# Kernel tuning notes

Hardware: AMD Instinct MI355X
Metric: run time of the kernel (lower is better)

## Reference

```python
import jax, jax.numpy as jnp
import numpy as np

T_STEPS = 16384  # sequence length T
N_DIM = 256      # input channels n
M_DIM = 512      # hidden/reservoir size m
K_MEM = 511      # memory rows K (addresses are 0..K, row 0 = 'no memory op')
L_OUT = 256      # output dims L


def setup_inputs() -> dict:
    key = jax.random.key(0)
    ks = jax.random.split(key, 10)
    s_ih = 1.0 / np.sqrt(N_DIM)
    s_hh = 1.0 / np.sqrt(M_DIM)
    X = jax.random.normal(ks[0], (T_STEPS, N_DIM), jnp.float32)
    h0 = jnp.zeros((M_DIM,), jnp.float32)  # init_state = zeros(m)
    # torch.nn.GRU parameters (single layer): weight_ih [3m, n], weight_hh [3m, m]
    W_ih = jax.random.normal(ks[1], (3 * M_DIM, N_DIM), jnp.float32) * s_ih
    W_hh = jax.random.normal(ks[2], (3 * M_DIM, M_DIM), jnp.float32) * s_hh
    b_ih = jax.random.normal(ks[3], (3 * M_DIM,), jnp.float32) * s_hh
    b_hh = jax.random.normal(ks[4], (3 * M_DIM,), jnp.float32) * s_hh
    # C_: Linear(m, K+1) -> memory address logits
    C_w = jax.random.normal(ks[5], (K_MEM + 1, M_DIM), jnp.float32) * s_hh
    C_b = jax.random.normal(ks[6], (K_MEM + 1,), jnp.float32) * s_hh
    # V_: Linear(m, L) -> outputs
    V_w = jax.random.normal(ks[7], (L_OUT, M_DIM), jnp.float32) * s_hh
    V_b = jax.random.normal(ks[8], (L_OUT,), jnp.float32) * s_hh
    return {"X": X, "h0": h0, "W_ih": W_ih, "W_hh": W_hh, "b_ih": b_ih,
            "b_hh": b_hh, "C_w": C_w, "C_b": C_b, "V_w": V_w, "V_b": V_b}


def reference(X, h0, W_ih, W_hh, b_ih, b_hh, C_w, C_b, V_w, V_b):
    m = h0.shape[0]
    n_addr = C_b.shape[0]  # K + 1

    def step(carry, x):
        h, M, written = carry
        # GRU cell (torch semantics)
        gi = W_ih @ x + b_ih          # [3m]
        gh = W_hh @ h + b_hh          # [3m]
        i_r, i_z, i_n = jnp.split(gi, 3)
        h_r, h_z, h_n = jnp.split(gh, 3)
        r = jax.nn.sigmoid(i_r + h_r)
        z = jax.nn.sigmoid(i_z + h_z)
        ng = jnp.tanh(i_n + r * h_n)
        h_new = (1.0 - z) * ng + z * h
        # discrete memory addressing via argmax over C_(h)
        logits = C_w @ h_new + C_b    # [K+1]
        q = jnp.argmax(logits)
        mem_q = M[q]                  # gather (read before write)
        has_entry = written[q] & (q > 0)
        # if address already written: read memory, replacing h
        h_out = jnp.where(has_entry, mem_q, h_new)
        # if address new (and > 0): write h into memory
        do_write = (q > 0) & jnp.logical_not(written[q])
        write_val = jnp.where(do_write, h_new, mem_q)  # no-op write otherwise
        M = M.at[q].set(write_val)
        written = written.at[q].set(written[q] | (q > 0))
        return (h_out, M, written), h_out

    M0 = jnp.zeros((n_addr, m), X.dtype)       # q_0 = 0 -> memory starts empty
    written0 = jnp.zeros((n_addr,), jnp.bool_)
    _, H = jax.lax.scan(step, (h0, M0, written0), X)  # H: [T, m]
    Y = H @ V_w.T + V_b                          # [T, L]
    return Y
```

## Files before the change

### kernel.cpp

```cpp
#include <hip/hip_runtime.h>
#include <stdint.h>

#define T_STEPS 16384
#define NDIM 256
#define MDIM 512
#define KP1 512
#define LOUT 256
#define G 16
#define TPB 256
#define NBLK 256

typedef unsigned long long u64;
typedef unsigned int u32;

constexpr size_t OFF_GH    = 0;
constexpr size_t OFF_GHS   = 512ull * 1536;
constexpr size_t OFF_M     = OFF_GHS + 1536;
constexpr size_t OFF_RING  = OFF_M + 512ull * 512;
constexpr size_t OFF_H     = OFF_RING + 4ull * 1536;
constexpr size_t OFF_VWT   = OFF_H + 16384ull * 512;
constexpr size_t OFF_FLAGS = OFF_VWT + 512ull * 256;

__device__ __forceinline__ float ld_cohf(const float* p) {
  return __hip_atomic_load(p, __ATOMIC_RELAXED, __HIP_MEMORY_SCOPE_AGENT);
}
__device__ __forceinline__ void st_cohf(float* p, float v) {
  __hip_atomic_store(p, v, __ATOMIC_RELAXED, __HIP_MEMORY_SCOPE_AGENT);
}
__device__ __forceinline__ u64 ld_flag(const u64* p) {
  return __hip_atomic_load(p, __ATOMIC_RELAXED, __HIP_MEMORY_SCOPE_AGENT);
}
__device__ __forceinline__ void st_flag_rel(u64* p, u64 v) {
  __hip_atomic_store(p, v, __ATOMIC_RELEASE, __HIP_MEMORY_SCOPE_AGENT);
}
__device__ __forceinline__ void st_flag_rlx(u64* p, u64 v) {
  __hip_atomic_store(p, v, __ATOMIC_RELAXED, __HIP_MEMORY_SCOPE_AGENT);
}

__device__ __forceinline__ u64 ld64_sc0(const u64* p) {
  u64 v;
  asm volatile("global_load_dwordx2 %0, %1, off sc0\n\t"
               "s_waitcnt vmcnt(0)"
               : "=&v"(v) : "v"(p) : "memory");
  return v;
}
__device__ __forceinline__ void st64_sc0(u64* p, u64 v) {
  asm volatile("global_store_dwordx2 %0, %1, off sc0" :: "v"(p), "v"(v) : "memory");
}
__device__ __forceinline__ void drain_vm() {
  asm volatile("s_waitcnt vmcnt(0)" ::: "memory");
}

#define HWREG_XCC_ID ((31u << 11) | 20u)
__device__ __forceinline__ u32 xcc_id() {
  return (u32)__builtin_amdgcn_s_getreg(HWREG_XCC_ID) & 0xFu;
}

__device__ __forceinline__ float sigm(float x) {
  return __builtin_amdgcn_rcpf(1.0f + __expf(-x));
}
__device__ __forceinline__ float tanh_(float x) {
  return 1.0f - 2.0f * __builtin_amdgcn_rcpf(__expf(2.0f * x) + 1.0f);
}

template<int CTRL>
__device__ __forceinline__ u32 dppmax(u32 v) {
  u32 t = (u32)__builtin_amdgcn_update_dpp(0, (int)v, CTRL, 0xf, 0xf, true);
  return v > t ? v : t;
}
__device__ __forceinline__ u32 wave_max_u32(u32 v) {
  v = dppmax<0x111>(v);
  v = dppmax<0x112>(v);
  v = dppmax<0x114>(v);
  v = dppmax<0x118>(v);
  v = dppmax<0x142>(v);
  v = dppmax<0x143>(v);
  return (u32)__builtin_amdgcn_readlane((int)v, 63);
}
__device__ __forceinline__ u32 row16_max_u32(u32 v) {
  v = dppmax<0x111>(v);
  v = dppmax<0x112>(v);
  v = dppmax<0x114>(v);
  v = dppmax<0x118>(v);
  return (u32)__builtin_amdgcn_readlane((int)v, 15);
}

__global__ __launch_bounds__(TPB, 1) void dmm_main(
    const float* __restrict__ X, const float* __restrict__ h0,
    const float* __restrict__ W_ih, const float* __restrict__ W_hh,
    const float* __restrict__ b_ih, const float* __restrict__ b_hh,
    const float* __restrict__ C_w, const float* __restrict__ C_b,
    float* __restrict__ ws)
{
  const int tid = threadIdx.x;
  const int w   = tid >> 6;
  const int l   = tid & 63;

  float* GH   = ws + OFF_GH;
  float* GHS  = ws + OFF_GHS;
  float* Mrow = ws + OFF_M;
  float* RING = ws + OFF_RING;
  float* H    = ws + OFF_H;
  u64*   F    = (u64*)(ws + OFF_FLAGS);

  u32* Ecnt = (u32*)Mrow;
  u64* Tst  = (u64*)(Mrow + 16);
  u64* Md   = (u64*)(Mrow + 64);

  __shared__ __align__(16) float hnew[MDIM];
  __shared__ __align__(16) float red[96 * 36];
  __shared__ u32 written[KP1];
  __shared__ u32 bcw;
  __shared__ int s_i;

  if (tid == 0) {
    u32 xcc = xcc_id();
    int widx = -1;
    if (xcc == 0) {
      u32 r = __hip_atomic_fetch_add(Ecnt, 1u, __ATOMIC_RELAXED,
                                     __HIP_MEMORY_SCOPE_AGENT);
      if (r < (u32)G) widx = (int)r;
    } else if (blockIdx.x < G) {
      int guard = 0; u32 c;
      do {
        c = __hip_atomic_load(Ecnt, __ATOMIC_RELAXED, __HIP_MEMORY_SCOPE_AGENT);
      } while (c < (u32)G && ++guard < (1 << 12));
      if (c < (u32)G) {
        u32 r = __hip_atomic_fetch_add(Ecnt, 1u, __ATOMIC_RELAXED,
                                       __HIP_MEMORY_SCOPE_AGENT);
        if (r < (u32)G) widx = (int)r;
      }
    }
    s_i = widx;
  }
  __syncthreads();
  const int b = s_i;
  __syncthreads();
  if (b < 0) return;

  __shared__ int s_good;
  if (tid == 0) s_good = 1;
  __syncthreads();
  for (int r = 1; r <= 8; ++r) {
    if (tid == 0 && s_good) {
      drain_vm();
      st64_sc0(&Tst[b], (u64)r);
    }
    if (w == 0 && s_good) {
      int guard = 0;
      for (;;) {
        u64 v = (u64)r;
        if (l < G) v = ld64_sc0(&Tst[l]);
        bool ok = (l >= G) || (v >= (u64)r);
        if (__ballot((int)ok) == ~0ull) break;
        if (++guard > (1 << 12)) { if (l == 0) s_good = 0; break; }
      }
    }
    __syncthreads();
  }
  if (tid == 0)
    __hip_atomic_store(&Md[b], 2ull | (u64)s_good, __ATOMIC_RELEASE,
                       __HIP_MEMORY_SCOPE_AGENT);
  if (w == 0) {
    int guard = 0, moderes = 0;
    for (;;) {
      u64 v = 3ull;
      if (l < G) v = __hip_atomic_load(&Md[l], __ATOMIC_ACQUIRE,
                                       __HIP_MEMORY_SCOPE_AGENT);
      bool ok = (l >= G) || ((v & 2ull) != 0);
      if (__ballot((int)ok) == ~0ull) {
        u64 bm = __ballot((int)((v & 1ull) != 0));
        moderes = (bm == ~0ull) ? 1 : 0;
        break;
      }
      if (++guard > (1 << 20)) { moderes = 0; break; }
    }
    if (l == 0) s_i = moderes;
  }
  __syncthreads();
  const bool SC0F = (s_i != 0);
  const int GSTEP = SC0F ? (1 << 12) : (1 << 22);


  const int pw   = (w >= 1) ? (w - 1) : 0;
  const int rloc = pw * 32 + (l >> 4) * 8;
  float wih[8][16];
  {
    int rbase = 96 * b + rloc;
    int cbase = 16 * (l & 15);
#pragma unroll
    for (int i = 0; i < 8; i++)
#pragma unroll
      for (int k = 0; k < 16; k++)
        wih[i][k] = W_ih[(size_t)(rbase + i) * NDIM + cbase + k];
  }
  float bihr[8];
#pragma unroll
  for (int i = 0; i < 8; i++) bihr[i] = b_ih[96 * b + rloc + i];

  float cw[4][16];
  {
    int rbase = 32 * b + w * 8 + (l >> 5) * 4;
    int cbase = 16 * (l & 31);
#pragma unroll
    for (int i = 0; i < 4; i++)
#pragma unroll
      for (int k = 0; k < 16; k++)
        cw[i][k] = C_w[(size_t)(rbase + i) * MDIM + cbase + k];
  }

  for (int i = tid; i < KP1; i += TPB) written[i] = 0u;
  if (tid == 0) bcw = 0u;
  hnew[tid]       = h0[tid];
  hnew[tid + 256] = h0[tid + 256];
  __syncthreads();

  float xreg[16];
  auto prefetchX = [&](int s) {
    int cbase = 16 * (l & 15);
#pragma unroll
    for (int k = 0; k < 16; k++) xreg[k] = X[(size_t)s * NDIM + cbase + k];
  };

  auto produce_gi = [&](int s) {
    float p[8];
#pragma unroll
    for (int i = 0; i < 8; i++) {
      float a = 0.f;
#pragma unroll
      for (int k = 0; k < 16; k++) a = fmaf(wih[i][k], xreg[k], a);
      p[i] = a;
    }
#pragma unroll
    for (int off = 1; off <= 8; off <<= 1) {
#pragma unroll
      for (int i = 0; i < 8; i++) p[i] += __shfl_xor(p[i], off, 64);
    }
    if ((l & 15) == 0) {
      float* dst = &RING[(size_t)(s & 3) * 1536 + 96 * b + rloc];
#pragma unroll
      for (int i = 0; i < 8; i++) st_cohf(&dst[i], p[i] + bihr[i]);
    }
  };

  auto compute_gh = [&](float* dst) {
    int cb = 16 * (l & 31);
    float hr[16];
#pragma unroll
    for (int k = 0; k < 16; k += 4) *(float4*)&hr[k] = *(const float4*)&hnew[cb + k];
    int rb = 96 * b + w * 24 + (l >> 5) * 12;
    float p[12];
#pragma unroll
    for (int i = 0; i < 12; i++) {
      float a = 0.f;
      const float* wr = &W_hh[(size_t)(rb + i) * MDIM + cb];
#pragma unroll
      for (int k = 0; k < 16; k++) a = fmaf(wr[k], hr[k], a);
      p[i] = a;
    }
    int rl = w * 24 + (l >> 5) * 12;
    int lc = l & 31;
#pragma unroll
    for (int i = 0; i < 12; i++) red[(rl + i) * 36 + lc] = p[i];
    __syncthreads();
    if (tid < 96) {
      float a = 0.f;
#pragma unroll
      for (int k = 0; k < 32; k += 4) {
        float4 v = *(const float4*)&red[tid * 36 + k];
        a += v.x + v.y + v.z + v.w;
      }
      a += b_hh[96 * b + tid];
      st_cohf(&dst[96 * b + tid], a);
    }
    __syncthreads();
  };

  if (w >= 1) {
    prefetchX(0); produce_gi(0);
    prefetchX(1); produce_gi(1);
    prefetchX(2); produce_gi(2);
    prefetchX(3);
  }
  __syncthreads();
  compute_gh(GHS);
  if (tid == 0) st_flag_rel(&F[b], 1ull);
  if (w == 0) {
    int guard = 0;
    for (;;) {
      u64 v = (l < G) ? ld_flag(&F[l]) : 1ull;
      if (__ballot((int)(v == 1ull)) == ~0ull) break;
      if (++guard > (1 << 22)) break;
    }
  }
  __syncthreads();

  const float* ghsrc = GHS;
  bool prevReadHit = false;
  int  qprev = 0;

  for (int t = 0; t < T_STEPS; ++t) {
    float g0 = ld_cohf(&ghsrc[tid]);
    float g1 = ld_cohf(&ghsrc[tid + 256]);
    float g2 = ld_cohf(&ghsrc[512 + tid]);
    float g3 = ld_cohf(&ghsrc[512 + tid + 256]);
    float g4 = ld_cohf(&ghsrc[1024 + tid]);
    float g5 = ld_cohf(&ghsrc[1024 + tid + 256]);
    float m0 = 0.f, m1 = 0.f;
    if (prevReadHit) {
      m0 = ld_cohf(&Mrow[(size_t)qprev * 512 + tid]);
      m1 = ld_cohf(&Mrow[(size_t)qprev * 512 + tid + 256]);
    }
    const float* gi = &RING[(size_t)(t & 3) * 1536];
    float i0 = ld_cohf(&gi[tid]);
    float i1 = ld_cohf(&gi[tid + 256]);
    float i2 = ld_cohf(&gi[512 + tid]);
    float i3 = ld_cohf(&gi[512 + tid + 256]);
    float i4 = ld_cohf(&gi[1024 + tid]);
    float i5 = ld_cohf(&gi[1024 + tid + 256]);

    if (prevReadHit && b == 0) {
      __builtin_nontemporal_store(m0, &H[(size_t)(t - 1) * 512 + tid]);
      __builtin_nontemporal_store(m1, &H[(size_t)(t - 1) * 512 + tid + 256]);
    }

    float hp0 = prevReadHit ? m0 : hnew[tid];
    float hp1 = prevReadHit ? m1 : hnew[tid + 256];
    float r0 = sigm(i0 + g0), r1 = sigm(i1 + g1);
    float z0 = sigm(i2 + g2), z1 = sigm(i3 + g3);
    float n0 = tanh_(fmaf(r0, g4, i4)), n1 = tanh_(fmaf(r1, g5, i5));
    float hn0 = fmaf(z0, hp0 - n0, n0);
    float hn1 = fmaf(z1, hp1 - n1, n1);
    hnew[tid]       = hn0;
    hnew[tid + 256] = hn1;
    __syncthreads();

    {
      int cb = 16 * (l & 31);
      float hr[16];
#pragma unroll
      for (int k = 0; k < 16; k += 4) *(float4*)&hr[k] = *(const float4*)&hnew[cb + k];
      float p0 = 0.f, p1 = 0.f, p2 = 0.f, p3 = 0.f;
#pragma unroll
      for (int k = 0; k < 16; k++) {
        p0 = fmaf(cw[0][k], hr[k], p0);
        p1 = fmaf(cw[1][k], hr[k], p1);
        p2 = fmaf(cw[2][k], hr[k], p2);
        p3 = fmaf(cw[3][k], hr[k], p3);
      }
      int rl = w * 8 + (l >> 5) * 4;
      int lc = l & 31;
      red[(rl + 0) * 36 + lc] = p0;
      red[(rl + 1) * 36 + lc] = p1;
      red[(rl + 2) * 36 + lc] = p2;
      red[(rl + 3) * 36 + lc] = p3;
    }
    __syncthreads();

    u64 ownkey = 0;
    if (w <= 1) {
      u32 ord = 0;
      if (l < 32) {
        const float4* rp = (const float4*)&red[l * 36];
        float4 v0 = rp[0], v1 = rp[1], v2 = rp[2], v3 = rp[3];
        float4 v4 = rp[4], v5 = rp[5], v6 = rp[6], v7 = rp[7];
        double d0 = ((double)v0.x + (double)v0.y) + ((double)v0.z + (double)v0.w);
        double d1 = ((double)v1.x + (double)v1.y) + ((double)v1.z + (double)v1.w);
        double d2 = ((double)v2.x + (double)v2.y) + ((double)v2.z + (double)v2.w);
        double d3 = ((double)v3.x + (double)v3.y) + ((double)v3.z + (double)v3.w);
        double d4 = ((double)v4.x + (double)v4.y) + ((double)v4.z + (double)v4.w);
        double d5 = ((double)v5.x + (double)v5.y) + ((double)v5.z + (double)v5.w);
        double d6 = ((double)v6.x + (double)v6.y) + ((double)v6.z + (double)v6.w);
        double d7 = ((double)v7.x + (double)v7.y) + ((double)v7.z + (double)v7.w);
        double a = (((d0 + d1) + (d2 + d3)) + ((d4 + d5) + (d6 + d7)))
                 + (double)C_b[32 * b + l];
        float af = (float)a;
        u32 bits = __float_as_uint(af);
        ord = (bits & 0x80000000u) ? ~bits : (bits | 0x80000000u);
      }
      u32 maxord = wave_max_u32(ord);
      u64 mask = __ballot((int)(ord == maxord));
      int lane = __builtin_ctzll(mask);
      u64 key41 = ((u64)maxord << 9) | (u64)(511 - (32 * b + lane));
      if (tid == 64) {
        u64 fv = ((u64)(t + 1) << 41) | key41;
        u64* fp = &F[16 + (size_t)(t & 1) * 16 + b];
        if (SC0F) st64_sc0(fp, fv); else st_flag_rlx(fp, fv);
      }
      ownkey = key41;
    }

    if (w >= 1 && t + 3 < T_STEPS) {
      produce_gi(t + 3);
      if (t + 4 < T_STEPS) prefetchX(t + 4);
    }

    u32 info;
    if (w == 0) {
      const bool need = (l < G) && (l != b);
      const u64* fp = &F[16 + (size_t)(t & 1) * 16 + l];
      u64 v = 0;
      if (SC0F) {
        int guard = 0;
        for (;;) {
          if (need) v = ld64_sc0(fp);
          bool ok = !need || ((v >> 41) == (u64)(t + 1));
          if (__ballot((int)ok) == ~0ull) break;
          if (++guard > GSTEP) break;
        }
      } else {
        u64 vp = need ? ld_flag(fp) : 0;
        int guard = 0;
        for (;;) {
          u64 vn = need ? ld_flag(fp) : 0;
          bool ok = !need || ((vp >> 41) == (u64)(t + 1));
          if (__ballot((int)ok) == ~0ull) { v = vp; break; }
          vp = vn;
          if (++guard > GSTEP) { v = vp; break; }
        }
      }
      u64 key = (l < G) ? ((l == b) ? ownkey : (v & ((1ull << 41) - 1))) : 0;
      u32 o = (u32)(key >> 9);
      u32 maxo = row16_max_u32(o);
      u32 cand = (o == maxo && l < G) ? (u32)(key & 511u) : 0u;
      u32 best = row16_max_u32(cand);
      int q = 511 - (int)best;
      u32 vinfo = 0;
      if (l == 0) {
        u32 wr = written[q];
        u32 fresh = (q > 0 && wr == 0u) ? 1u : 0u;
        u32 rhit  = (q > 0 && wr != 0u) ? 1u : 0u;
        if (fresh) written[q] = 1u;
        vinfo = (u32)q | (fresh << 16) | (rhit << 17);
      }
      vinfo = (u32)__builtin_amdgcn_readfirstlane((int)vinfo);
      info = vinfo;
      if (l == 0)
        __hip_atomic_store(&bcw, (vinfo << 4) | ((u32)(t + 1) & 0xFu),
                           __ATOMIC_RELEASE, __HIP_MEMORY_SCOPE_WORKGROUP);
    } else {
      u32 v;
      int guard = 0;
      for (;;) {
        v = __hip_atomic_load(&bcw, __ATOMIC_ACQUIRE, __HIP_MEMORY_SCOPE_WORKGROUP);
        if ((v & 0xFu) == ((u32)(t + 1) & 0xFu)) break;
        if (++guard > (1 << 25)) break;
      }
      info = v >> 4;
    }
    int  q     = (int)(info & 0xFFFFu);
    bool fresh = (info >> 16) & 1u;
    bool rhit  = (info >> 17) & 1u;

    if (!rhit) {
      if (b == 0) {
        __builtin_nontemporal_store(hnew[tid], &H[(size_t)t * 512 + tid]);
        __builtin_nontemporal_store(hnew[tid + 256], &H[(size_t)t * 512 + tid + 256]);
      }
      float* dst;
      if (fresh) {
        if (tid < 32) st_cohf(&Mrow[(size_t)q * 512 + 32 * b + tid], hnew[32 * b + tid]);
        dst = &GH[(size_t)q * 1536];
      } else {
        dst = GHS;
      }
      compute_gh(dst);
      if (tid == 0) {
        u64* fp = &F[48 + (size_t)(t & 1) * 16 + b];
        if (SC0F) { drain_vm(); st64_sc0(fp, (u64)(t + 1)); }
        else st_flag_rel(fp, (u64)(t + 1));
      }
      if (w == 0) {
        int guard = 0;
        for (;;) {
          u64 v;
          const u64* fp = &F[48 + (size_t)(t & 1) * 16 + l];
          if (l < G) v = SC0F ? ld64_sc0(fp) : ld_flag(fp);
          else v = (u64)(t + 1);
          bool ok = (l >= G) || (v == (u64)(t + 1));
          if (__ballot((int)ok) == ~0ull) break;
          if (++guard > GSTEP) break;
        }
      }
      __syncthreads();
      ghsrc = dst;
      prevReadHit = false;
    } else {
      ghsrc = &GH[(size_t)q * 1536];
      prevReadHit = true;
      qprev = q;
    }
  }

  if (prevReadHit && b == 0) {
    float a = ld_cohf(&Mrow[(size_t)qprev * 512 + tid]);
    float c = ld_cohf(&Mrow[(size_t)qprev * 512 + tid + 256]);
    __builtin_nontemporal_store(a, &H[(size_t)(T_STEPS - 1) * 512 + tid]);
    __builtin_nontemporal_store(c, &H[(size_t)(T_STEPS - 1) * 512 + tid + 256]);
  }
}

__global__ void vw_transpose(const float* __restrict__ Vw, float* __restrict__ VwT) {
  int idx = blockIdx.x * 256 + threadIdx.x;
  if (blockIdx.x == 0) {
    float* M0 = VwT - (OFF_VWT - OFF_M);
    M0[threadIdx.x] = 0.f;
  }
  int kk = idx >> 8, ll = idx & 255;
  VwT[idx] = Vw[(size_t)ll * MDIM + kk];
}

__global__ __launch_bounds__(256) void y_gemm(const float* __restrict__ Hm,
                                              const float* __restrict__ VwT,
                                              const float* __restrict__ Vb,
                                              float* __restrict__ Y) {
  int t0 = blockIdx.x * 16;
  int tid = threadIdx.x;
  __shared__ __align__(16) float hs[16 * MDIM];
  for (int i = tid; i < 16 * MDIM; i += 256)
    hs[i] = Hm[(size_t)t0 * MDIM + i];
  __syncthreads();
  float acc[16];
  float vb = Vb[tid];
#pragma unroll
  for (int r = 0; r < 16; r++) acc[r] = vb;
  for (int k = 0; k < MDIM; k += 4) {
    float v0 = VwT[(size_t)(k + 0) * LOUT + tid];
    float v1 = VwT[(size_t)(k + 1) * LOUT + tid];
    float v2 = VwT[(size_t)(k + 2) * LOUT + tid];
    float v3 = VwT[(size_t)(k + 3) * LOUT + tid];
#pragma unroll
    for (int r = 0; r < 16; r++) {
      float4 h4 = *(const float4*)&hs[r * MDIM + k];
      acc[r] = fmaf(h4.x, v0, fmaf(h4.y, v1, fmaf(h4.z, v2, fmaf(h4.w, v3, acc[r]))));
    }
  }
#pragma unroll
  for (int r = 0; r < 16; r++)
    Y[(size_t)(t0 + r) * LOUT + tid] = acc[r];
}

extern "C" void kernel_launch(void* const* d_in, const int* in_sizes, int n_in,
                              void* d_out, int out_size, void* d_ws, size_t ws_size,
                              hipStream_t stream) {
  const float* X    = (const float*)d_in[0];
  const float* h0   = (const float*)d_in[1];
  const float* W_ih = (const float*)d_in[2];
  const float* W_hh = (const float*)d_in[3];
  const float* b_ih = (const float*)d_in[4];
  const float* b_hh = (const float*)d_in[5];
  const float* C_w  = (const float*)d_in[6];
  const float* C_b  = (const float*)d_in[7];
  const float* V_w  = (const float*)d_in[8];
  const float* V_b  = (const float*)d_in[9];
  float* ws  = (float*)d_ws;
  float* VwT = ws + OFF_VWT;
  float* Hm  = ws + OFF_H;

  hipLaunchKernelGGL(vw_transpose, dim3(512), dim3(256), 0, stream, V_w, VwT);
  hipLaunchKernelGGL(dmm_main, dim3(NBLK), dim3(TPB), 0, stream,
                     X, h0, W_ih, W_hh, b_ih, b_hh, C_w, C_b, ws);
  hipLaunchKernelGGL(y_gemm, dim3(T_STEPS / 16), dim3(256), 0, stream,
                     Hm, VwT, V_b, (float*)d_out);
}
```

Baseline: 40.87 ms.

## Use sc0 inline-asm loads/stores and padded flag slots for cross-block sync

On the SC0F path, the per-step loads of gate and memory rows are bundled into one inline-asm block of sc0 loads with a single waitcnt, and stores use sc0 stores followed by explicit drains. The argmax and completion flags move to padded slots (stride 16 u64) placed in the otherwise-unused GH row 0 region, which vw_transpose now zeroes. X prefetches become nontemporal loads. The aim is to cut coherence latency and false sharing in the per-step inter-block handshakes, at the cost of relying on ordering assumptions for the sc0 cache-bypass semantics and extra vmcnt drains.

```diff
diff --git a/kernel.cpp b/kernel.cpp
--- a/kernel.cpp
+++ b/kernel.cpp
@@ -47,9 +47,35 @@
 __device__ __forceinline__ void st64_sc0(u64* p, u64 v) {
   asm volatile("global_store_dwordx2 %0, %1, off sc0" :: "v"(p), "v"(v) : "memory");
 }
+__device__ __forceinline__ void stf_sc0(float* p, float v) {
+  asm volatile("global_store_dword %0, %1, off sc0" :: "v"(p), "v"(v) : "memory");
+}
 __device__ __forceinline__ void drain_vm() {
   asm volatile("s_waitcnt vmcnt(0)" ::: "memory");
 }
+
+#define BUNDLE_SC0()                                                 \
+      asm volatile(                                                  \
+        "global_load_dword %0, %14, off sc0\n\t"                     \
+        "global_load_dword %1, %14, off offset:1024 sc0\n\t"         \
+        "global_load_dword %2, %14, off offset:2048 sc0\n\t"         \
+        "global_load_dword %3, %14, off offset:3072 sc0\n\t"         \
+        "global_load_dword %4, %15, off sc0\n\t"                     \
+        "global_load_dword %5, %15, off offset:1024 sc0\n\t"         \
+        "global_load_dword %6, %16, off sc0\n\t"                     \
+        "global_load_dword %7, %16, off offset:1024 sc0\n\t"         \
+        "global_load_dword %8, %16, off offset:2048 sc0\n\t"         \
+        "global_load_dword %9, %16, off offset:3072 sc0\n\t"         \
+        "global_load_dword %10, %17, off sc0\n\t"                    \
+        "global_load_dword %11, %17, off offset:1024 sc0\n\t"        \
+        "global_load_dword %12, %18, off sc0\n\t"                    \
+        "global_load_dword %13, %18, off offset:1024 sc0\n\t"        \
+        "s_waitcnt vmcnt(0)"                                         \
+        : "=&v"(g0), "=&v"(g1), "=&v"(g2), "=&v"(g3), "=&v"(g4), "=&v"(g5), \
+          "=&v"(i0), "=&v"(i1), "=&v"(i2), "=&v"(i3), "=&v"(i4), "=&v"(i5), \
+          "=&v"(m0), "=&v"(m1)                                       \
+        : "v"(pg0), "v"(pg4), "v"(pi0), "v"(pi4), "v"(pm0)           \
+        : "memory")
 
 #define HWREG_XCC_ID ((31u << 11) | 20u)
 __device__ __forceinline__ u32 xcc_id() {
@@ -102,6 +128,8 @@
   float* RING = ws + OFF_RING;
   float* H    = ws + OFF_H;
   u64*   F    = (u64*)(ws + OFF_FLAGS);
+  u64*   FB1  = (u64*)(ws + OFF_GH);
+  u64*   FC1  = (u64*)(ws + OFF_GH) + 512;
 
   u32* Ecnt = (u32*)Mrow;
   u64* Tst  = (u64*)(Mrow + 16);
@@ -218,8 +246,14 @@
   float xreg[16];
   auto prefetchX = [&](int s) {
     int cbase = 16 * (l & 15);
-#pragma unroll
-    for (int k = 0; k < 16; k++) xreg[k] = X[(size_t)s * NDIM + cbase + k];
+    const float* xp = &X[(size_t)s * NDIM + cbase];
+    if (SC0F) {
+#pragma unroll
+      for (int k = 0; k < 16; k++) xreg[k] = __builtin_nontemporal_load(&xp[k]);
+    } else {
+#pragma unroll
+      for (int k = 0; k < 16; k++) xreg[k] = xp[k];
+    }
   };
 
   auto produce_gi = [&](int s) {
@@ -238,8 +272,13 @@
     }
     if ((l & 15) == 0) {
       float* dst = &RING[(size_t)(s & 3) * 1536 + 96 * b + rloc];
-#pragma unroll
-      for (int i = 0; i < 8; i++) st_cohf(&dst[i], p[i] + bihr[i]);
+      if (SC0F) {
+#pragma unroll
+        for (int i = 0; i < 8; i++) stf_sc0(&dst[i], p[i] + bihr[i]);
+      } else {
+#pragma unroll
+        for (int i = 0; i < 8; i++) st_cohf(&dst[i], p[i] + bihr[i]);
+      }
     }
   };
 
@@ -271,8 +310,10 @@
         a += v.x + v.y + v.z + v.w;
       }
       a += b_hh[96 * b + tid];
-      st_cohf(&dst[96 * b + tid], a);
-    }
+      if (SC0F) stf_sc0(&dst[96 * b + tid], a);
+      else      st_cohf(&dst[96 * b + tid], a);
+    }
+    if (SC0F) drain_vm();
     __syncthreads();
   };
 
@@ -300,24 +341,34 @@
   int  qprev = 0;
 
   for (int t = 0; t < T_STEPS; ++t) {
-    float g0 = ld_cohf(&ghsrc[tid]);
-    float g1 = ld_cohf(&ghsrc[tid + 256]);
-    float g2 = ld_cohf(&ghsrc[512 + tid]);
-    float g3 = ld_cohf(&ghsrc[512 + tid + 256]);
-    float g4 = ld_cohf(&ghsrc[1024 + tid]);
-    float g5 = ld_cohf(&ghsrc[1024 + tid + 256]);
-    float m0 = 0.f, m1 = 0.f;
-    if (prevReadHit) {
-      m0 = ld_cohf(&Mrow[(size_t)qprev * 512 + tid]);
-      m1 = ld_cohf(&Mrow[(size_t)qprev * 512 + tid + 256]);
-    }
     const float* gi = &RING[(size_t)(t & 3) * 1536];
-    float i0 = ld_cohf(&gi[tid]);
-    float i1 = ld_cohf(&gi[tid + 256]);
-    float i2 = ld_cohf(&gi[512 + tid]);
-    float i3 = ld_cohf(&gi[512 + tid + 256]);
-    float i4 = ld_cohf(&gi[1024 + tid]);
-    float i5 = ld_cohf(&gi[1024 + tid + 256]);
+    float g0, g1, g2, g3, g4, g5, i0, i1, i2, i3, i4, i5, m0, m1;
+    if (SC0F) {
+      const float* pg0 = ghsrc + tid;
+      const float* pg4 = ghsrc + 1024 + tid;
+      const float* pi0 = gi + tid;
+      const float* pi4 = gi + 1024 + tid;
+      const float* pm0 = Mrow + (size_t)qprev * 512 + tid;
+      BUNDLE_SC0();
+    } else {
+      g0 = ld_cohf(&ghsrc[tid]);
+      g1 = ld_cohf(&ghsrc[tid + 256]);
+      g2 = ld_cohf(&ghsrc[512 + tid]);
+      g3 = ld_cohf(&ghsrc[512 + tid + 256]);
+      g4 = ld_cohf(&ghsrc[1024 + tid]);
+      g5 = ld_cohf(&ghsrc[1024 + tid + 256]);
+      m0 = 0.f; m1 = 0.f;
+      if (prevReadHit) {
+        m0 = ld_cohf(&Mrow[(size_t)qprev * 512 + tid]);
+        m1 = ld_cohf(&Mrow[(size_t)qprev * 512 + tid + 256]);
+      }
+      i0 = ld_cohf(&gi[tid]);
+      i1 = ld_cohf(&gi[tid + 256]);
+      i2 = ld_cohf(&gi[512 + tid]);
+      i3 = ld_cohf(&gi[512 + tid + 256]);
+      i4 = ld_cohf(&gi[1024 + tid]);
+      i5 = ld_cohf(&gi[1024 + tid + 256]);
+    }
 
     if (prevReadHit && b == 0) {
       __builtin_nontemporal_store(m0, &H[(size_t)(t - 1) * 512 + tid]);
@@ -384,23 +435,24 @@
       u64 key41 = ((u64)maxord << 9) | (u64)(511 - (32 * b + lane));
       if (tid == 64) {
         u64 fv = ((u64)(t + 1) << 41) | key41;
-        u64* fp = &F[16 + (size_t)(t & 1) * 16 + b];
-        if (SC0F) st64_sc0(fp, fv); else st_flag_rlx(fp, fv);
+        if (SC0F) st64_sc0(&FB1[((size_t)(t & 1) * 16 + b) * 16], fv);
+        else      st_flag_rlx(&F[16 + (size_t)(t & 1) * 16 + b], fv);
       }
       ownkey = key41;
     }
 
     if (w >= 1 && t + 3 < T_STEPS) {
       produce_gi(t + 3);
+      if (SC0F) drain_vm();
       if (t + 4 < T_STEPS) prefetchX(t + 4);
     }
 
     u32 info;
     if (w == 0) {
       const bool need = (l < G) && (l != b);
-      const u64* fp = &F[16 + (size_t)(t & 1) * 16 + l];
       u64 v = 0;
       if (SC0F) {
+        const u64* fp = &FB1[((size_t)(t & 1) * 16 + l) * 16];
         int guard = 0;
         for (;;) {
           if (need) v = ld64_sc0(fp);
@@ -409,6 +461,7 @@
           if (++guard > GSTEP) break;
         }
       } else {
+        const u64* fp = &F[16 + (size_t)(t & 1) * 16 + l];
         u64 vp = need ? ld_flag(fp) : 0;
         int guard = 0;
         for (;;) {
@@ -459,24 +512,28 @@
       }
       float* dst;
       if (fresh) {
-        if (tid < 32) st_cohf(&Mrow[(size_t)q * 512 + 32 * b + tid], hnew[32 * b + tid]);
+        if (tid < 32) {
+          float* mp = &Mrow[(size_t)q * 512 + 32 * b + tid];
+          if (SC0F) stf_sc0(mp, hnew[32 * b + tid]);
+          else      st_cohf(mp, hnew[32 * b + tid]);
+        }
         dst = &GH[(size_t)q * 1536];
       } else {
         dst = GHS;
       }
       compute_gh(dst);
       if (tid == 0) {
-        u64* fp = &F[48 + (size_t)(t & 1) * 16 + b];
-        if (SC0F) { drain_vm(); st64_sc0(fp, (u64)(t + 1)); }
-        else st_flag_rel(fp, (u64)(t + 1));
+        if (SC0F) st64_sc0(&FC1[(size_t)b * 16], (u64)(t + 1));
+        else      st_flag_rel(&F[48 + (size_t)(t & 1) * 16 + b], (u64)(t + 1));
       }
       if (w == 0) {
         int guard = 0;
         for (;;) {
-          u64 v;
-          const u64* fp = &F[48 + (size_t)(t & 1) * 16 + l];
-          if (l < G) v = SC0F ? ld64_sc0(fp) : ld_flag(fp);
-          else v = (u64)(t + 1);
+          u64 v = (u64)(t + 1);
+          if (l < G) {
+            if (SC0F) v = ld64_sc0(&FC1[(size_t)l * 16]);
+            else      v = ld_flag(&F[48 + (size_t)(t & 1) * 16 + l]);
+          }
           bool ok = (l >= G) || (v == (u64)(t + 1));
           if (__ballot((int)ok) == ~0ull) break;
           if (++guard > GSTEP) break;
@@ -493,8 +550,18 @@
   }
 
   if (prevReadHit && b == 0) {
-    float a = ld_cohf(&Mrow[(size_t)qprev * 512 + tid]);
-    float c = ld_cohf(&Mrow[(size_t)qprev * 512 + tid + 256]);
+    float a, c;
+    if (SC0F) {
+      const float* pm = Mrow + (size_t)qprev * 512 + tid;
+      asm volatile(
+        "global_load_dword %0, %2, off sc0\n\t"
+        "global_load_dword %1, %2, off offset:1024 sc0\n\t"
+        "s_waitcnt vmcnt(0)"
+        : "=&v"(a), "=&v"(c) : "v"(pm) : "memory");
+    } else {
+      a = ld_cohf(&Mrow[(size_t)qprev * 512 + tid]);
+      c = ld_cohf(&Mrow[(size_t)qprev * 512 + tid + 256]);
+    }
     __builtin_nontemporal_store(a, &H[(size_t)(T_STEPS - 1) * 512 + tid]);
     __builtin_nontemporal_store(c, &H[(size_t)(T_STEPS - 1) * 512 + tid + 256]);
   }
@@ -505,6 +572,12 @@
   if (blockIdx.x == 0) {
     float* M0 = VwT - (OFF_VWT - OFF_M);
     M0[threadIdx.x] = 0.f;
+    M0[threadIdx.x + 256] = 0.f;
+  }
+  if (blockIdx.x == 1) {
+    float* G0 = VwT - OFF_VWT;
+#pragma unroll
+    for (int i = 0; i < 6; i++) G0[threadIdx.x + 256 * i] = 0.f;
   }
   int kk = idx >> 8, ll = idx & 255;
   VwT[idx] = Vw[(size_t)ll * MDIM + kk];
```

Result: slower. 42.28 ms (+3.4%).

## Pad cross-block flags onto separate lines and pipeline flag polling loads

Applied to the files above, without the earlier changes.

Moves the per-step argmax and gh-completion flags into padded slots, one per 128-byte stride, inside the otherwise unused GH row 0, so blocks do not share cache lines when polling. The argmax flag poll keeps two sc0 loads in flight with vmcnt(1) waits, which cuts the round-trip latency of each spin iteration. It also makes X prefetches nontemporal and drops the drain before the completion flag store. It zero-initializes the new flag area in the transpose kernel, and it relies on GH row 0 never being used as data, since q>0 for every write.

```diff
diff --git a/kernel.cpp b/kernel.cpp
--- a/kernel.cpp
+++ b/kernel.cpp
@@ -102,6 +102,8 @@
   float* RING = ws + OFF_RING;
   float* H    = ws + OFF_H;
   u64*   F    = (u64*)(ws + OFF_FLAGS);
+  u64*   FB1  = (u64*)(ws + OFF_GH);
+  u64*   FC1  = (u64*)(ws + OFF_GH) + 512;
 
   u32* Ecnt = (u32*)Mrow;
   u64* Tst  = (u64*)(Mrow + 16);
@@ -218,8 +220,14 @@
   float xreg[16];
   auto prefetchX = [&](int s) {
     int cbase = 16 * (l & 15);
-#pragma unroll
-    for (int k = 0; k < 16; k++) xreg[k] = X[(size_t)s * NDIM + cbase + k];
+    const float* xp = &X[(size_t)s * NDIM + cbase];
+    if (SC0F) {
+#pragma unroll
+      for (int k = 0; k < 16; k++) xreg[k] = __builtin_nontemporal_load(&xp[k]);
+    } else {
+#pragma unroll
+      for (int k = 0; k < 16; k++) xreg[k] = xp[k];
+    }
   };
 
   auto produce_gi = [&](int s) {
@@ -384,8 +392,8 @@
       u64 key41 = ((u64)maxord << 9) | (u64)(511 - (32 * b + lane));
       if (tid == 64) {
         u64 fv = ((u64)(t + 1) << 41) | key41;
-        u64* fp = &F[16 + (size_t)(t & 1) * 16 + b];
-        if (SC0F) st64_sc0(fp, fv); else st_flag_rlx(fp, fv);
+        if (SC0F) st64_sc0(&FB1[((size_t)(t & 1) * 16 + b) * 16], fv);
+        else      st_flag_rlx(&F[16 + (size_t)(t & 1) * 16 + b], fv);
       }
       ownkey = key41;
     }
@@ -398,17 +406,34 @@
     u32 info;
     if (w == 0) {
       const bool need = (l < G) && (l != b);
-      const u64* fp = &F[16 + (size_t)(t & 1) * 16 + l];
       u64 v = 0;
       if (SC0F) {
+        drain_vm();
+        const u64* fp = &FB1[((size_t)(t & 1) * 16 + l) * 16];
+        u64 va = 0, vb = 0;
+        if (need)
+          asm volatile("global_load_dwordx2 %0, %2, off sc0\n\t"
+                       "global_load_dwordx2 %1, %2, off sc0"
+                       : "=&v"(va), "=&v"(vb) : "v"(fp) : "memory");
         int guard = 0;
         for (;;) {
-          if (need) v = ld64_sc0(fp);
-          bool ok = !need || ((v >> 41) == (u64)(t + 1));
-          if (__ballot((int)ok) == ~0ull) break;
-          if (++guard > GSTEP) break;
+          asm volatile("s_waitcnt vmcnt(1)" ::: "memory");
+          bool ok = !need || ((va >> 41) == (u64)(t + 1));
+          if (__ballot((int)ok) == ~0ull) { v = va; break; }
+          if (need)
+            asm volatile("global_load_dwordx2 %0, %1, off sc0"
+                         : "=&v"(va) : "v"(fp) : "memory");
+          asm volatile("s_waitcnt vmcnt(1)" ::: "memory");
+          ok = !need || ((vb >> 41) == (u64)(t + 1));
+          if (__ballot((int)ok) == ~0ull) { v = vb; break; }
+          if (need)
+            asm volatile("global_load_dwordx2 %0, %1, off sc0"
+                         : "=&v"(vb) : "v"(fp) : "memory");
+          if (++guard > GSTEP) { v = va; break; }
         }
+        drain_vm();
       } else {
+        const u64* fp = &F[16 + (size_t)(t & 1) * 16 + l];
         u64 vp = need ? ld_flag(fp) : 0;
         int guard = 0;
         for (;;) {
@@ -466,17 +491,17 @@
       }
       compute_gh(dst);
       if (tid == 0) {
-        u64* fp = &F[48 + (size_t)(t & 1) * 16 + b];
-        if (SC0F) { drain_vm(); st64_sc0(fp, (u64)(t + 1)); }
-        else st_flag_rel(fp, (u64)(t + 1));
+        if (SC0F) st64_sc0(&FC1[(size_t)b * 16], (u64)(t + 1));
+        else      st_flag_rel(&F[48 + (size_t)(t & 1) * 16 + b], (u64)(t + 1));
       }
       if (w == 0) {
         int guard = 0;
         for (;;) {
-          u64 v;
-          const u64* fp = &F[48 + (size_t)(t & 1) * 16 + l];
-          if (l < G) v = SC0F ? ld64_sc0(fp) : ld_flag(fp);
-          else v = (u64)(t + 1);
+          u64 v = (u64)(t + 1);
+          if (l < G) {
+            if (SC0F) v = ld64_sc0(&FC1[(size_t)l * 16]);
+            else      v = ld_flag(&F[48 + (size_t)(t & 1) * 16 + l]);
+          }
           bool ok = (l >= G) || (v == (u64)(t + 1));
           if (__ballot((int)ok) == ~0ull) break;
           if (++guard > GSTEP) break;
@@ -505,6 +530,12 @@
   if (blockIdx.x == 0) {
     float* M0 = VwT - (OFF_VWT - OFF_M);
     M0[threadIdx.x] = 0.f;
+    M0[threadIdx.x + 256] = 0.f;
+  }
+  if (blockIdx.x == 1) {
+    float* G0 = VwT - OFF_VWT;
+#pragma unroll
+    for (int i = 0; i < 6; i++) G0[threadIdx.x + 256 * i] = 0.f;
   }
   int kk = idx >> 8, ll = idx & 255;
   VwT[idx] = Vw[(size_t)ll * MDIM + kk];
```

New measurement: 36.65 ms. 10.3% less time.
